# Kernel tuning notes

Measured on AMD Instinct MI355X. Metric: run time of the kernel, lower is better.

Reference implementation:

```python
import jax, jax.numpy as jnp
import numpy as np

N_NODES = 100000
N_EDGES = 1600000
IN_DIM, HID_DIM, OUT_DIM = 128, 128, 64


def setup_inputs() -> dict:
    key = jax.random.key(0)
    k1, k2, k3, k4 = jax.random.split(key, 4)
    x = jax.random.normal(k1, (N_NODES, IN_DIM), dtype=jnp.float32)
    edge_index = jax.random.randint(k2, (2, N_EDGES), 0, N_NODES, dtype=jnp.int32)
    # Glorot-ish init for weights
    W1 = jax.random.normal(k3, (IN_DIM, HID_DIM), dtype=jnp.float32) / np.sqrt(IN_DIM)
    W2 = jax.random.normal(k4, (HID_DIM, OUT_DIM), dtype=jnp.float32) / np.sqrt(HID_DIM)
    b1 = jnp.zeros((HID_DIM,), dtype=jnp.float32)
    b2 = jnp.zeros((OUT_DIM,), dtype=jnp.float32)
    return {"x": x, "edge_index": edge_index, "W1": W1, "b1": b1, "W2": W2, "b2": b2}


def _gcn_norm(edge_index, num_nodes):
    # PyG gcn_norm: add self-loops, symmetric normalization deg^-1/2 A deg^-1/2
    loops = jnp.arange(num_nodes, dtype=edge_index.dtype)
    src = jnp.concatenate([edge_index[0], loops])  # [E+N]
    tgt = jnp.concatenate([edge_index[1], loops])
    deg = jax.ops.segment_sum(jnp.ones_like(tgt, dtype=jnp.float32), tgt,
                              num_segments=num_nodes)
    dinv = jnp.where(deg > 0, jax.lax.rsqrt(deg), 0.0)
    norm = dinv[src] * dinv[tgt]  # [E+N]
    return src, tgt, norm


def _gcn_conv(x, W, b, src, tgt, norm, num_nodes):
    h = x @ W                              # [N, D_out] transform first (GCNConv order)
    msg = norm[:, None] * h[src]           # gather + scale per edge
    agg = jax.ops.segment_sum(msg, tgt, num_segments=num_nodes)  # scatter-add
    return agg + b


def reference(x, edge_index, W1, b1, W2, b2):
    n = x.shape[0]
    src, tgt, norm = _gcn_norm(edge_index, n)
    h = jax.nn.relu(_gcn_conv(x, W1, b1, src, tgt, norm, n))
    out = _gcn_conv(h, W2, b2, src, tgt, norm, n)
    return out
```

## Files before the change

### kernel.cpp

```cpp
#include <hip/hip_runtime.h>


typedef unsigned int uint;
typedef unsigned short ushort;
typedef __attribute__((ext_vector_type(8))) short bf16x8;
typedef __attribute__((ext_vector_type(8))) ushort u16x8;
typedef __attribute__((ext_vector_type(4))) float f32x4;

#define BSHIFT 8
#define MAXBK  512
#define NB     256
#define CAP    8192

__device__ inline ushort f2bf(float f) {
    uint u = __float_as_uint(f);
    return (ushort)((u + 0x7fffu + ((u >> 16) & 1u)) >> 16);
}
__device__ inline float bf_lo(uint u) { return __uint_as_float(u << 16); }
__device__ inline float bf_hi(uint u) { return __uint_as_float(u & 0xffff0000u); }

__global__ __launch_bounds__(256) void hist_kernel(const int* __restrict__ tgt,
                                                   int* __restrict__ counts,
                                                   int E, int chunk, int nbk) {
    __shared__ int hist[MAXBK];
    int t = threadIdx.x, b = blockIdx.x;
    for (int i = t; i < nbk; i += 256) hist[i] = 0;
    __syncthreads();
    int s = b * chunk, e = min(E, s + chunk);
    int i = s + t * 4;
    for (; i + 3 < e; i += 1024) {
        int4 tv = *(const int4*)&tgt[i];
        atomicAdd(&hist[tv.x >> BSHIFT], 1);
        atomicAdd(&hist[tv.y >> BSHIFT], 1);
        atomicAdd(&hist[tv.z >> BSHIFT], 1);
        atomicAdd(&hist[tv.w >> BSHIFT], 1);
    }
    if (i < e)
        for (int k = i; k < e; ++k) atomicAdd(&hist[tgt[k] >> BSHIFT], 1);
    __syncthreads();
    for (int i2 = t; i2 < nbk; i2 += 256) counts[i2 * NB + b] = hist[i2];
}

__global__ __launch_bounds__(256) void scan_partial(const int* __restrict__ in,
                                                    int* __restrict__ bsum, int M) {
    int t = threadIdx.x, b = blockIdx.x;
    int base = b * 1024 + t * 4;
    int s = 0;
#pragma unroll
    for (int k = 0; k < 4; ++k) s += (base + k < M) ? in[base + k] : 0;
#pragma unroll
    for (int off = 32; off > 0; off >>= 1) s += __shfl_down(s, off, 64);
    __shared__ int ws[4];
    if ((t & 63) == 0) ws[t >> 6] = s;
    __syncthreads();
    if (t == 0) bsum[b] = ws[0] + ws[1] + ws[2] + ws[3];
}

__global__ __launch_bounds__(256) void scan_final_counts(int* __restrict__ counts,
                                                         const int* __restrict__ bsum,
                                                         int M) {
    int t = threadIdx.x, b = blockIdx.x;
    int lane = t & 63, wid = t >> 6;
    int p = 0;
    for (int i = t; i < b; i += 256) p += bsum[i];
#pragma unroll
    for (int off = 32; off > 0; off >>= 1) p += __shfl_down(p, off, 64);
    __shared__ int ps[4];
    if (lane == 0) ps[wid] = p;
    __syncthreads();
    int pre = ps[0] + ps[1] + ps[2] + ps[3];

    int base = b * 1024 + t * 4;
    int d[4];
#pragma unroll
    for (int k = 0; k < 4; ++k) d[k] = (base + k < M) ? counts[base + k] : 0;
    int tot = d[0] + d[1] + d[2] + d[3];
    int incl = tot;
#pragma unroll
    for (int off = 1; off < 64; off <<= 1) {
        int u = __shfl_up(incl, off, 64);
        if (lane >= off) incl += u;
    }
    __shared__ int wsum[4];
    if (lane == 63) wsum[wid] = incl;
    __syncthreads();
    int woff = 0;
    for (int w = 0; w < wid; ++w) woff += wsum[w];
    int run = incl - tot + woff + pre;
#pragma unroll
    for (int k = 0; k < 4; ++k) {
        if (base + k < M) counts[base + k] = run;
        run += d[k];
    }
}

__global__ __launch_bounds__(256) void bucket_scatter(const int* __restrict__ src,
                                                      const int* __restrict__ tgt,
                                                      const int* __restrict__ offsets,
                                                      int* __restrict__ tmpP,
                                                      int E, int chunk, int nbk) {
    __shared__ int cur[MAXBK];
    int t = threadIdx.x, b = blockIdx.x;
    for (int i = t; i < nbk; i += 256) cur[i] = offsets[i * NB + b];
    __syncthreads();
    int s = b * chunk, e = min(E, s + chunk);
    int i = s + t * 4;
    for (; i + 3 < e; i += 1024) {
        int4 sv = *(const int4*)&src[i];
        int4 tv = *(const int4*)&tgt[i];
        int p0 = atomicAdd(&cur[tv.x >> BSHIFT], 1);
        tmpP[p0] = (sv.x << BSHIFT) | (tv.x & 255);
        int p1 = atomicAdd(&cur[tv.y >> BSHIFT], 1);
        tmpP[p1] = (sv.y << BSHIFT) | (tv.y & 255);
        int p2 = atomicAdd(&cur[tv.z >> BSHIFT], 1);
        tmpP[p2] = (sv.z << BSHIFT) | (tv.z & 255);
        int p3 = atomicAdd(&cur[tv.w >> BSHIFT], 1);
        tmpP[p3] = (sv.w << BSHIFT) | (tv.w & 255);
    }
    if (i < e) {
        for (int k = i; k < e; ++k) {
            int tg = tgt[k];
            int p = atomicAdd(&cur[tg >> BSHIFT], 1);
            tmpP[p] = (src[k] << BSHIFT) | (tg & 255);
        }
    }
}

__global__ __launch_bounds__(256) void bucket_finish(const int* __restrict__ tmpP,
                                                     const int* __restrict__ offsets,
                                                     int* __restrict__ rowptr,
                                                     float* __restrict__ dinv,
                                                     int* __restrict__ csr_src,
                                                     int N, int E, int nbk) {
    __shared__ int stage[CAP];
    __shared__ int cnt[256];
    __shared__ int wsum[4];
    int t = threadIdx.x, b = blockIdx.x;
    cnt[t] = 0;
    __syncthreads();
    int s = offsets[b * NB];
    int e = (b + 1 < nbk) ? offsets[(b + 1) * NB] : E;
    int m = e - s;
    for (int i = t; i < m; i += 256) {
        int ed = tmpP[s + i];
        if (i < CAP) stage[i] = ed;
        atomicAdd(&cnt[ed & 255], 1);
    }
    __syncthreads();
    int lane = t & 63, wid = t >> 6;
    int d = cnt[t];
    int incl = d;
#pragma unroll
    for (int off = 1; off < 64; off <<= 1) {
        int u = __shfl_up(incl, off, 64);
        if (lane >= off) incl += u;
    }
    if (lane == 63) wsum[wid] = incl;
    __syncthreads();
    int woff = 0;
    for (int w = 0; w < wid; ++w) woff += wsum[w];
    int excl = s + incl - d + woff;
    int node = b * 256 + t;
    if (node < N) {
        rowptr[node] = excl;
        dinv[node] = rsqrtf((float)d + 1.0f);
    }
    if (b == nbk - 1 && t == 255) rowptr[N] = E;
    cnt[t] = excl;
    __syncthreads();
    for (int i = t; i < m; i += 256) {
        int ed = (i < CAP) ? stage[i] : tmpP[s + i];
        int p = atomicAdd(&cnt[ed & 255], 1);
        csr_src[p] = ed >> BSHIFT;
    }
}

template <int M, typename AT>
__global__ __launch_bounds__(256) void gemm_mfma(const AT* __restrict__ A,
                                                 const float* __restrict__ W,
                                                 const float* __restrict__ dinv,
                                                 ushort* __restrict__ C, int N) {
    constexpr int WTS = 136;
    __shared__ ushort WT[M * WTS];
    const int tid = threadIdx.x;
    for (int i = tid; i < 128 * (M / 4); i += 256) {
        int k = i / (M / 4);
        int n0 = (i % (M / 4)) * 4;
        float4 w = *(const float4*)&W[k * M + n0];
        WT[(n0 + 0) * WTS + k] = f2bf(w.x);
        WT[(n0 + 1) * WTS + k] = f2bf(w.y);
        WT[(n0 + 2) * WTS + k] = f2bf(w.z);
        WT[(n0 + 3) * WTS + k] = f2bf(w.w);
    }
    __syncthreads();

    const int wv = tid >> 6, lane = tid & 63;
    const int quad = lane >> 4, mrow = lane & 15;
    int arow_i = blockIdx.x * 64 + wv * 16 + mrow;
    if (arow_i >= N) arow_i = N - 1;
    const AT* arow = &A[(size_t)arow_i * 128];

    f32x4 acc[M / 16];
#pragma unroll
    for (int t = 0; t < M / 16; ++t) acc[t] = (f32x4){0.f, 0.f, 0.f, 0.f};

#pragma unroll
    for (int ks = 0; ks < 4; ++ks) {
        const int k0 = ks * 32 + quad * 8;
        bf16x8 af;
        if constexpr (sizeof(AT) == 4) {
            float4 a0 = *(const float4*)&arow[k0];
            float4 a1 = *(const float4*)&arow[k0 + 4];
            af[0] = (short)f2bf(a0.x); af[1] = (short)f2bf(a0.y);
            af[2] = (short)f2bf(a0.z); af[3] = (short)f2bf(a0.w);
            af[4] = (short)f2bf(a1.x); af[5] = (short)f2bf(a1.y);
            af[6] = (short)f2bf(a1.z); af[7] = (short)f2bf(a1.w);
        } else {
            af = *(const bf16x8*)&arow[k0];
        }
#pragma unroll
        for (int t = 0; t < M / 16; ++t) {
            int n = t * 16 + mrow;
            bf16x8 bfr = *(const bf16x8*)&WT[n * WTS + k0];
            acc[t] = __builtin_amdgcn_mfma_f32_16x16x32_bf16(af, bfr, acc[t], 0, 0, 0);
        }
    }

    const int orow0 = blockIdx.x * 64 + wv * 16 + quad * 4;
#pragma unroll
    for (int r = 0; r < 4; ++r) {
        int orow = orow0 + r;
        if (orow < N) {
            float dv = dinv[orow];
#pragma unroll
            for (int t = 0; t < M / 16; ++t)
                C[(size_t)orow * M + t * 16 + mrow] = f2bf(dv * acc[t][r]);
        }
    }
}

template <int D, bool RELU, bool OUTBF>
__global__ __launch_bounds__(256) void gather_kernel(
    const ushort* __restrict__ h, const int* __restrict__ rowptr,
    const int* __restrict__ csr_src, const float* __restrict__ dinv,
    const float* __restrict__ bias, void* __restrict__ outv, int N) {
    constexpr int Q = D / 8;
    constexpr int G = 64 / Q;
    const int wid = threadIdx.x >> 6, lane = threadIdx.x & 63;
    const int node = blockIdx.x * 4 + wid;
    if (node >= N) return;
    const int g = lane / Q, q = lane % Q;
    const int qoff = q * 8;
    const int beg = rowptr[node], end = rowptr[node + 1];
    float acc[8] = {};

    for (int j = beg; j < end; j += 2 * G) {
        int e0 = j + g, e1 = j + G + g;
        {
            bool v = e0 < end;
            int s = v ? csr_src[e0] : node;
            float m = v ? 1.0f : 0.0f;
            uint4 hv = *(const uint4*)&h[(size_t)s * D + qoff];
            acc[0] += m * bf_lo(hv.x); acc[1] += m * bf_hi(hv.x);
            acc[2] += m * bf_lo(hv.y); acc[3] += m * bf_hi(hv.y);
            acc[4] += m * bf_lo(hv.z); acc[5] += m * bf_hi(hv.z);
            acc[6] += m * bf_lo(hv.w); acc[7] += m * bf_hi(hv.w);
        }
        {
            bool v = e1 < end;
            int s = v ? csr_src[e1] : node;
            float m = v ? 1.0f : 0.0f;
            uint4 hv = *(const uint4*)&h[(size_t)s * D + qoff];
            acc[0] += m * bf_lo(hv.x); acc[1] += m * bf_hi(hv.x);
            acc[2] += m * bf_lo(hv.y); acc[3] += m * bf_hi(hv.y);
            acc[4] += m * bf_lo(hv.z); acc[5] += m * bf_hi(hv.z);
            acc[6] += m * bf_lo(hv.w); acc[7] += m * bf_hi(hv.w);
        }
    }
#pragma unroll
    for (int m2 = Q; m2 < 64; m2 <<= 1)
#pragma unroll
        for (int k = 0; k < 8; ++k) acc[k] += __shfl_xor(acc[k], m2, 64);

    {
        uint4 hv = *(const uint4*)&h[(size_t)node * D + qoff];
        acc[0] += bf_lo(hv.x); acc[1] += bf_hi(hv.x);
        acc[2] += bf_lo(hv.y); acc[3] += bf_hi(hv.y);
        acc[4] += bf_lo(hv.z); acc[5] += bf_hi(hv.z);
        acc[6] += bf_lo(hv.w); acc[7] += bf_hi(hv.w);
    }
    if (g == 0) {
        const float di = dinv[node];
        float4 b0 = *(const float4*)&bias[qoff];
        float4 b1 = *(const float4*)&bias[qoff + 4];
        float r[8] = {di * acc[0] + b0.x, di * acc[1] + b0.y,
                      di * acc[2] + b0.z, di * acc[3] + b0.w,
                      di * acc[4] + b1.x, di * acc[5] + b1.y,
                      di * acc[6] + b1.z, di * acc[7] + b1.w};
        if (RELU) {
#pragma unroll
            for (int k = 0; k < 8; ++k) r[k] = fmaxf(r[k], 0.0f);
        }
        if constexpr (OUTBF) {
            ushort* out = (ushort*)outv;
            u16x8 o;
#pragma unroll
            for (int k = 0; k < 8; ++k) o[k] = f2bf(r[k]);
            *(u16x8*)&out[(size_t)node * D + qoff] = o;
        } else {
            float* out = (float*)outv;
            *(float4*)&out[(size_t)node * D + qoff]     = make_float4(r[0], r[1], r[2], r[3]);
            *(float4*)&out[(size_t)node * D + qoff + 4] = make_float4(r[4], r[5], r[6], r[7]);
        }
    }
}

extern "C" void kernel_launch(void* const* d_in, const int* in_sizes, int n_in,
                              void* d_out, int out_size, void* d_ws, size_t ws_size,
                              hipStream_t stream) {
    const float* x  = (const float*)d_in[0];
    const int*   ei = (const int*)d_in[1];
    const float* W1 = (const float*)d_in[2];
    const float* b1 = (const float*)d_in[3];
    const float* W2 = (const float*)d_in[4];
    const float* b2 = (const float*)d_in[5];
    float* out = (float*)d_out;

    const int N = in_sizes[0] / 128;
    const int E = in_sizes[1] / 2;
    const int* src = ei;
    const int* tgt = ei + E;

    const int nbk   = (N + 255) >> BSHIFT;
    const int chunk = (((E + NB - 1) / NB) + 3) & ~3;
    const int Mc    = nbk * NB;

    float* ws = (float*)d_ws;
    const size_t Np = (size_t)((N + 3) & ~3);
    float*  dinv    = ws;
    int*    rowptr  = (int*)(ws + Np);
    int*    counts  = rowptr + Np + 4;
    int*    bsum    = counts + MAXBK * NB;
    int*    csr_src = bsum + 128;
    int*    tmpP    = csr_src + E;
    ushort* h       = (ushort*)(tmpP + E);
    ushort* h1      = h + (size_t)N * 128;
    ushort* h2      = h;

    const int nbc = (Mc + 1023) / 1024;

    hist_kernel<<<NB, 256, 0, stream>>>(tgt, counts, E, chunk, nbk);
    scan_partial<<<nbc, 256, 0, stream>>>(counts, bsum, Mc);
    scan_final_counts<<<nbc, 256, 0, stream>>>(counts, bsum, Mc);
    bucket_scatter<<<NB, 256, 0, stream>>>(src, tgt, counts, tmpP, E, chunk, nbk);
    bucket_finish<<<nbk, 256, 0, stream>>>(tmpP, counts, rowptr, dinv, csr_src, N, E, nbk);

    gemm_mfma<128, float><<<(N + 63) / 64, 256, 0, stream>>>(x, W1, dinv, h, N);
    gather_kernel<128, true, true><<<(N + 3) / 4, 256, 0, stream>>>(
        h, rowptr, csr_src, dinv, b1, h1, N);

    gemm_mfma<64, ushort><<<(N + 63) / 64, 256, 0, stream>>>(h1, W2, dinv, h2, N);
    gather_kernel<64, false, false><<<(N + 3) / 4, 256, 0, stream>>>(
        h2, rowptr, csr_src, dinv, b2, out, N);
}
```

Baseline: 309.2 us.

## Store features in column-sliced layout and gather slice-by-slice per node block

Intermediate feature matrices are stored as 16-column slices ([D/16][N][16]) instead of row-major, and the gather kernel now processes 64 nodes per block, two threads per node, looping over slices so each slice (about 3.2MB) stays cache-resident during the random gathers. Block edge indices are staged in shared memory to avoid re-reading csr_src for each slice. This trades per-node warp parallelism for better L2 locality; high-degree nodes now run serially in one thread pair, which risks load imbalance and lower memory-level parallelism.

Result: slower. 343.3 us (+11.0%).

```diff
diff --git a/kernel.cpp b/kernel.cpp
--- a/kernel.cpp
+++ b/kernel.cpp
@@ -198,7 +198,6 @@
     const int quad = lane >> 4, mrow = lane & 15;
     int arow_i = blockIdx.x * 64 + wv * 16 + mrow;
     if (arow_i >= N) arow_i = N - 1;
-    const AT* arow = &A[(size_t)arow_i * 128];
 
     f32x4 acc[M / 16];
 #pragma unroll
@@ -209,6 +208,7 @@
         const int k0 = ks * 32 + quad * 8;
         bf16x8 af;
         if constexpr (sizeof(AT) == 4) {
+            const float* arow = (const float*)A + (size_t)arow_i * 128;
             float4 a0 = *(const float4*)&arow[k0];
             float4 a1 = *(const float4*)&arow[k0 + 4];
             af[0] = (short)f2bf(a0.x); af[1] = (short)f2bf(a0.y);
@@ -216,7 +216,8 @@
             af[4] = (short)f2bf(a1.x); af[5] = (short)f2bf(a1.y);
             af[6] = (short)f2bf(a1.z); af[7] = (short)f2bf(a1.w);
         } else {
-            af = *(const bf16x8*)&arow[k0];
+            af = *(const bf16x8*)((const ushort*)A +
+                                  ((size_t)(k0 >> 4) * N + arow_i) * 16 + (k0 & 15));
         }
 #pragma unroll
         for (int t = 0; t < M / 16; ++t) {
@@ -234,85 +235,97 @@
             float dv = dinv[orow];
 #pragma unroll
             for (int t = 0; t < M / 16; ++t)
-                C[(size_t)orow * M + t * 16 + mrow] = f2bf(dv * acc[t][r]);
+                C[((size_t)t * N + orow) * 16 + mrow] = f2bf(dv * acc[t][r]);
         }
     }
 }
 
 template <int D, bool RELU, bool OUTBF>
-__global__ __launch_bounds__(256) void gather_kernel(
+__global__ __launch_bounds__(128) void gather_sliced(
     const ushort* __restrict__ h, const int* __restrict__ rowptr,
     const int* __restrict__ csr_src, const float* __restrict__ dinv,
     const float* __restrict__ bias, void* __restrict__ outv, int N) {
-    constexpr int Q = D / 8;
-    constexpr int G = 64 / Q;
-    const int wid = threadIdx.x >> 6, lane = threadIdx.x & 63;
-    const int node = blockIdx.x * 4 + wid;
-    if (node >= N) return;
-    const int g = lane / Q, q = lane % Q;
+    constexpr int NS = D / 16;
+    constexpr int CAPE = 2048;
+    __shared__ int eL[CAPE];
+    const int tid = threadIdx.x;
+    const int base = blockIdx.x * 64;
+    const int bbeg = rowptr[base];
+    const int bend = rowptr[min(base + 64, N)];
+    const int m = bend - bbeg;
+    for (int i = tid; i < m && i < CAPE; i += 128) eL[i] = csr_src[bbeg + i];
+    __syncthreads();
+
+    const int node = base + (tid >> 1);
+    const int q = tid & 1;
     const int qoff = q * 8;
-    const int beg = rowptr[node], end = rowptr[node + 1];
-    float acc[8] = {};
-
-    for (int j = beg; j < end; j += 2 * G) {
-        int e0 = j + g, e1 = j + G + g;
-        {
-            bool v = e0 < end;
-            int s = v ? csr_src[e0] : node;
-            float m = v ? 1.0f : 0.0f;
-            uint4 hv = *(const uint4*)&h[(size_t)s * D + qoff];
-            acc[0] += m * bf_lo(hv.x); acc[1] += m * bf_hi(hv.x);
-            acc[2] += m * bf_lo(hv.y); acc[3] += m * bf_hi(hv.y);
-            acc[4] += m * bf_lo(hv.z); acc[5] += m * bf_hi(hv.z);
-            acc[6] += m * bf_lo(hv.w); acc[7] += m * bf_hi(hv.w);
-        }
-        {
-            bool v = e1 < end;
-            int s = v ? csr_src[e1] : node;
-            float m = v ? 1.0f : 0.0f;
-            uint4 hv = *(const uint4*)&h[(size_t)s * D + qoff];
-            acc[0] += m * bf_lo(hv.x); acc[1] += m * bf_hi(hv.x);
-            acc[2] += m * bf_lo(hv.y); acc[3] += m * bf_hi(hv.y);
-            acc[4] += m * bf_lo(hv.z); acc[5] += m * bf_hi(hv.z);
-            acc[6] += m * bf_lo(hv.w); acc[7] += m * bf_hi(hv.w);
-        }
-    }
-#pragma unroll
-    for (int m2 = Q; m2 < 64; m2 <<= 1)
-#pragma unroll
-        for (int k = 0; k < 8; ++k) acc[k] += __shfl_xor(acc[k], m2, 64);
-
-    {
-        uint4 hv = *(const uint4*)&h[(size_t)node * D + qoff];
-        acc[0] += bf_lo(hv.x); acc[1] += bf_hi(hv.x);
-        acc[2] += bf_lo(hv.y); acc[3] += bf_hi(hv.y);
-        acc[4] += bf_lo(hv.z); acc[5] += bf_hi(hv.z);
-        acc[6] += bf_lo(hv.w); acc[7] += bf_hi(hv.w);
-    }
-    if (g == 0) {
-        const float di = dinv[node];
-        float4 b0 = *(const float4*)&bias[qoff];
-        float4 b1 = *(const float4*)&bias[qoff + 4];
-        float r[8] = {di * acc[0] + b0.x, di * acc[1] + b0.y,
-                      di * acc[2] + b0.z, di * acc[3] + b0.w,
-                      di * acc[4] + b1.x, di * acc[5] + b1.y,
-                      di * acc[6] + b1.z, di * acc[7] + b1.w};
-        if (RELU) {
-#pragma unroll
-            for (int k = 0; k < 8; ++k) r[k] = fmaxf(r[k], 0.0f);
-        }
-        if constexpr (OUTBF) {
-            ushort* out = (ushort*)outv;
-            u16x8 o;
-#pragma unroll
-            for (int k = 0; k < 8; ++k) o[k] = f2bf(r[k]);
-            *(u16x8*)&out[(size_t)node * D + qoff] = o;
-        } else {
-            float* out = (float*)outv;
-            *(float4*)&out[(size_t)node * D + qoff]     = make_float4(r[0], r[1], r[2], r[3]);
-            *(float4*)&out[(size_t)node * D + qoff + 4] = make_float4(r[4], r[5], r[6], r[7]);
-        }
-    }
+    const bool alive = node < N;
+    int beg = 0, end = 0;
+    float di = 0.f;
+    if (alive) {
+        beg = rowptr[node];
+        end = rowptr[node + 1];
+        di = dinv[node];
+    }
+
+    auto acc8 = [](float* a, uint4 v) {
+        a[0] += bf_lo(v.x); a[1] += bf_hi(v.x);
+        a[2] += bf_lo(v.y); a[3] += bf_hi(v.y);
+        a[4] += bf_lo(v.z); a[5] += bf_hi(v.z);
+        a[6] += bf_lo(v.w); a[7] += bf_hi(v.w);
+    };
+
+    auto run = [&](auto LD) {
+#pragma unroll 1
+        for (int s = 0; s < NS; ++s) {
+            const ushort* hs = h + (size_t)s * N * 16;
+            float acc[8] = {};
+            if (alive) {
+                int j = beg;
+                for (; j + 1 < end; j += 2) {
+                    int s0 = LD(j), s1 = LD(j + 1);
+                    uint4 va = *(const uint4*)&hs[(size_t)s0 * 16 + qoff];
+                    uint4 vb = *(const uint4*)&hs[(size_t)s1 * 16 + qoff];
+                    acc8(acc, va);
+                    acc8(acc, vb);
+                }
+                if (j < end) {
+                    int s0 = LD(j);
+                    acc8(acc, *(const uint4*)&hs[(size_t)s0 * 16 + qoff]);
+                }
+                acc8(acc, *(const uint4*)&hs[(size_t)node * 16 + qoff]);
+
+                float4 b0 = *(const float4*)&bias[s * 16 + qoff];
+                float4 b1 = *(const float4*)&bias[s * 16 + qoff + 4];
+                float r[8] = {di * acc[0] + b0.x, di * acc[1] + b0.y,
+                              di * acc[2] + b0.z, di * acc[3] + b0.w,
+                              di * acc[4] + b1.x, di * acc[5] + b1.y,
+                              di * acc[6] + b1.z, di * acc[7] + b1.w};
+                if (RELU) {
+#pragma unroll
+                    for (int k = 0; k < 8; ++k) r[k] = fmaxf(r[k], 0.0f);
+                }
+                if constexpr (OUTBF) {
+                    ushort* out = (ushort*)outv;
+                    u16x8 o;
+#pragma unroll
+                    for (int k = 0; k < 8; ++k) o[k] = f2bf(r[k]);
+                    *(u16x8*)&out[((size_t)s * N + node) * 16 + qoff] = o;
+                } else {
+                    float* out = (float*)outv;
+                    *(float4*)&out[(size_t)node * D + s * 16 + qoff] =
+                        make_float4(r[0], r[1], r[2], r[3]);
+                    *(float4*)&out[(size_t)node * D + s * 16 + qoff + 4] =
+                        make_float4(r[4], r[5], r[6], r[7]);
+                }
+            }
+        }
+    };
+
+    if (m <= CAPE)
+        run([&](int j) { return eL[j - bbeg]; });
+    else
+        run([&](int j) { return csr_src[j]; });
 }
 
 extern "C" void kernel_launch(void* const* d_in, const int* in_sizes, int n_in,
@@ -355,11 +368,13 @@
     bucket_scatter<<<NB, 256, 0, stream>>>(src, tgt, counts, tmpP, E, chunk, nbk);
     bucket_finish<<<nbk, 256, 0, stream>>>(tmpP, counts, rowptr, dinv, csr_src, N, E, nbk);
 
+    const int ngb = (N + 63) / 64;
+
     gemm_mfma<128, float><<<(N + 63) / 64, 256, 0, stream>>>(x, W1, dinv, h, N);
-    gather_kernel<128, true, true><<<(N + 3) / 4, 256, 0, stream>>>(
+    gather_sliced<128, true, true><<<ngb, 128, 0, stream>>>(
         h, rowptr, csr_src, dinv, b1, h1, N);
 
     gemm_mfma<64, ushort><<<(N + 63) / 64, 256, 0, stream>>>(h1, W2, dinv, h2, N);
-    gather_kernel<64, false, false><<<(N + 3) / 4, 256, 0, stream>>>(
+    gather_sliced<64, false, false><<<ngb, 128, 0, stream>>>(
         h2, rowptr, csr_src, dinv, b2, out, N);
 }
```
